# Kernel tuning notes

Measured on AMD Instinct MI355X. Metric: run time of the kernel, lower is better.

Reference implementation:

```python
import jax, jax.numpy as jnp
import numpy as np

TIME_STEP = 7
B, C, D, H, W = 1, 3, 128, 160, 128


def grid_sample_3d(vol, grid):
    """Trilinear grid_sample, padding_mode='border', align_corners=True.
    vol: [B,C,D,H,W]; grid: [B,D,H,W,3] with last dim (x,y,z) in [-1,1]."""
    b, c, d, h, w = vol.shape
    # unnormalize (align_corners=True) and clamp to volume (border padding)
    ix = jnp.clip((grid[..., 0] + 1.0) * 0.5 * (w - 1), 0.0, w - 1)
    iy = jnp.clip((grid[..., 1] + 1.0) * 0.5 * (h - 1), 0.0, h - 1)
    iz = jnp.clip((grid[..., 2] + 1.0) * 0.5 * (d - 1), 0.0, d - 1)

    x0f = jnp.floor(ix); y0f = jnp.floor(iy); z0f = jnp.floor(iz)
    wx = (ix - x0f).reshape(b, 1, -1)
    wy = (iy - y0f).reshape(b, 1, -1)
    wz = (iz - z0f).reshape(b, 1, -1)

    x0 = x0f.astype(jnp.int32); x1 = jnp.minimum(x0 + 1, w - 1)
    y0 = y0f.astype(jnp.int32); y1 = jnp.minimum(y0 + 1, h - 1)
    z0 = z0f.astype(jnp.int32); z1 = jnp.minimum(z0 + 1, d - 1)

    vol_flat = vol.reshape(b, c, d * h * w)

    def gather(zi, yi, xi):
        idx = ((zi * h + yi) * w + xi).reshape(b, 1, -1)  # [B,1,N]
        return jnp.take_along_axis(vol_flat, idx, axis=2)  # [B,C,N]

    out = (gather(z0, y0, x0) * (1 - wz) * (1 - wy) * (1 - wx)
         + gather(z0, y0, x1) * (1 - wz) * (1 - wy) * wx
         + gather(z0, y1, x0) * (1 - wz) * wy * (1 - wx)
         + gather(z0, y1, x1) * (1 - wz) * wy * wx
         + gather(z1, y0, x0) * wz * (1 - wy) * (1 - wx)
         + gather(z1, y0, x1) * wz * (1 - wy) * wx
         + gather(z1, y1, x0) * wz * wy * (1 - wx)
         + gather(z1, y1, x1) * wz * wy * wx)
    return out.reshape(b, c, d, h, w)


def setup_inputs() -> dict:
    key = jax.random.key(0)
    k1, = jax.random.split(key, 1)
    velocity = jax.random.normal(k1, (B, C, D, H, W), dtype=jnp.float32)
    # identity sampling grid, normalized to [-1,1], last dim order (x,y,z)
    gz, gy, gx = jnp.meshgrid(
        jnp.linspace(-1.0, 1.0, D, dtype=jnp.float32),
        jnp.linspace(-1.0, 1.0, H, dtype=jnp.float32),
        jnp.linspace(-1.0, 1.0, W, dtype=jnp.float32),
        indexing='ij')
    sample_grid = jnp.broadcast_to(jnp.stack([gx, gy, gz], axis=-1)[None], (B, D, H, W, 3))
    range_flow = jnp.asarray(0.4, dtype=jnp.float32)
    return {"velocity": velocity, "sample_grid": sample_grid, "range_flow": range_flow}


def reference(velocity, sample_grid, range_flow):
    flow = velocity / (2.0 ** TIME_STEP)
    for _ in range(TIME_STEP):
        grid = sample_grid + jnp.transpose(flow, (0, 2, 3, 4, 1)) * range_flow
        flow = flow + grid_sample_3d(flow, grid)
    return flow
```

## Files before the change

### kernel.cpp

```cpp
#include <hip/hip_runtime.h>


constexpr int D = 128, H = 160, W = 128;
constexpr int N = D * H * W;
constexpr int HC = H / 2, WC = W / 2;
constexpr int NBLK = (D / 2) * (H / 2) * (W / 64);
constexpr int NUM_XCD = 8;
constexpr int CHUNKS_PER_XCD = NBLK / NUM_XCD;

struct alignas(4) f2 { float a, b; };

__device__ __forceinline__ int cube_idx(int z, int y, int x) {
    return ((((z >> 1) * HC + (y >> 1)) * WC + (x >> 1)) << 3)
         | ((z & 1) << 2) | ((y & 1) << 1) | (x & 1);
}

template <bool SRC_PLANAR, bool DST_PLANAR>
__global__ __launch_bounds__(256)
void diffeo_step(const void* __restrict__ src_raw,
                 const float* __restrict__ rf_p,
                 void* __restrict__ dst_raw)
{
    const int b   = blockIdx.x;
    const int xcd = b & (NUM_XCD - 1);
    const int k   = b >> 3;
    const int vb  = xcd * CHUNKS_PER_XCD + k;

    const int zc  = vb / (HC * 2);
    const int rem = vb - zc * (HC * 2);
    const int yc  = rem >> 1;
    const int xh  = rem & 1;

    const int t = threadIdx.x;
    const int x = (xh << 6) | (t & 63);
    const int y = (yc << 1) | ((t >> 6) & 1);
    const int z = (zc << 1) | (t >> 7);

    const float rf = rf_p[0];
    const float s  = 1.0f / 128.0f;

    float3 f;
    if (SRC_PLANAR) {
        const float* sp = (const float*)src_raw;
        const int i = (z * H + y) * W + x;
        f = make_float3(sp[i] * s, sp[i + N] * s, sp[i + 2 * N] * s);
    } else {
        const float4 v = ((const float4*)src_raw)[cube_idx(z, y, x)];
        f = make_float3(v.x, v.y, v.z);
    }

    const float ix = fminf(fmaxf((float)x + f.x * (rf * 0.5f * (float)(W - 1)), 0.0f), (float)(W - 1));
    const float iy = fminf(fmaxf((float)y + f.y * (rf * 0.5f * (float)(H - 1)), 0.0f), (float)(H - 1));
    const float iz = fminf(fmaxf((float)z + f.z * (rf * 0.5f * (float)(D - 1)), 0.0f), (float)(D - 1));

    const float x0f = floorf(ix), y0f = floorf(iy), z0f = floorf(iz);
    const float wx = ix - x0f, wy = iy - y0f, wz = iz - z0f;
    const int x0 = (int)x0f, y0 = (int)y0f, z0 = (int)z0f;
    const int y1 = min(y0 + 1, H - 1);
    const int z1 = min(z0 + 1, D - 1);

    float3 p0[4], p1[4];

    if (SRC_PLANAR) {
        const float* sp = (const float*)src_raw;
        const int xb = min(x0, W - 2);
        const bool hix = (x0 == W - 1);
        int ofs[4];
        ofs[0] = (z0 * H + y0) * W + xb;
        ofs[1] = (z0 * H + y1) * W + xb;
        ofs[2] = (z1 * H + y0) * W + xb;
        ofs[3] = (z1 * H + y1) * W + xb;
#pragma unroll
        for (int q = 0; q < 4; ++q) {
            const f2 px = *(const f2*)(sp + ofs[q]);
            const f2 py = *(const f2*)(sp + N + ofs[q]);
            const f2 pz = *(const f2*)(sp + 2 * N + ofs[q]);
            p0[q] = make_float3(px.a * s, py.a * s, pz.a * s);
            p1[q] = make_float3(px.b * s, py.b * s, pz.b * s);
        }
        if (hix) {
#pragma unroll
            for (int q = 0; q < 4; ++q) p0[q] = p1[q];
        }
    } else {
        const float4* sc = (const float4*)src_raw;
        const int x1 = min(x0 + 1, W - 1);
#pragma unroll
        for (int q = 0; q < 4; ++q) {
            const int zi = (q & 2) ? z1 : z0;
            const int yi = (q & 1) ? y1 : y0;
            const float4 a  = sc[cube_idx(zi, yi, x0)];
            const float4 bq = sc[cube_idx(zi, yi, x1)];
            p0[q] = make_float3(a.x, a.y, a.z);
            p1[q] = make_float3(bq.x, bq.y, bq.z);
        }
    }

    const float omx = 1.0f - wx, omy = 1.0f - wy, omz = 1.0f - wz;
    const float w00 = omz * omy, w01 = omz * wy, w10 = wz * omy, w11 = wz * wy;

    const float vx = w00 * (omx * p0[0].x + wx * p1[0].x)
                   + w01 * (omx * p0[1].x + wx * p1[1].x)
                   + w10 * (omx * p0[2].x + wx * p1[2].x)
                   + w11 * (omx * p0[3].x + wx * p1[3].x);
    const float vy = w00 * (omx * p0[0].y + wx * p1[0].y)
                   + w01 * (omx * p0[1].y + wx * p1[1].y)
                   + w10 * (omx * p0[2].y + wx * p1[2].y)
                   + w11 * (omx * p0[3].y + wx * p1[3].y);
    const float vz = w00 * (omx * p0[0].z + wx * p1[0].z)
                   + w01 * (omx * p0[1].z + wx * p1[1].z)
                   + w10 * (omx * p0[2].z + wx * p1[2].z)
                   + w11 * (omx * p0[3].z + wx * p1[3].z);

    const float o0 = f.x + vx, o1 = f.y + vy, o2 = f.z + vz;

    if (DST_PLANAR) {
        float* __restrict__ dp = (float*)dst_raw;
        const int i = (z * H + y) * W + x;
        dp[i] = o0; dp[i + N] = o1; dp[i + 2 * N] = o2;
    } else {
        ((float4*)dst_raw)[cube_idx(z, y, x)] = make_float4(o0, o1, o2, 0.0f);
    }
}

extern "C" void kernel_launch(void* const* d_in, const int* in_sizes, int n_in,
                              void* d_out, int out_size, void* d_ws, size_t ws_size,
                              hipStream_t stream)
{
    const float* vel = (const float*)d_in[0];
    const float* rf  = (const float*)d_in[2];

    float4* A = (float4*)d_ws;
    float4* B = (float4*)((char*)d_ws + (size_t)48 * 1024 * 1024);

    const dim3 blk(256);
    const dim3 grd(NBLK);

    diffeo_step<true , false><<<grd, blk, 0, stream>>>(vel, rf, A);
    diffeo_step<false, false><<<grd, blk, 0, stream>>>(A,   rf, B);
    diffeo_step<false, false><<<grd, blk, 0, stream>>>(B,   rf, A);
    diffeo_step<false, false><<<grd, blk, 0, stream>>>(A,   rf, B);
    diffeo_step<false, false><<<grd, blk, 0, stream>>>(B,   rf, A);
    diffeo_step<false, false><<<grd, blk, 0, stream>>>(A,   rf, B);
    diffeo_step<false, true ><<<grd, blk, 0, stream>>>(B,   rf, d_out);
}
```

Baseline: 360.2 us.

## Replace Morton-cube float4 layout with linear packed float3 intermediate layout

Intermediate flow buffers change from a 2x2x2-cube-blocked float4 layout to a plain linear array of packed float3. Each 256-thread block now covers a contiguous run of voxels, and the gathers index by linear offset with x and x+1 as adjacent elements. This cuts per-voxel storage from 16 to 12 bytes and drops the cube index arithmetic, at the cost of unaligned 12-byte accesses and less locality in y and z for the trilinear neighbours. The final planar output now uses nontemporal stores.

```diff
diff --git a/kernel.cpp b/kernel.cpp
--- a/kernel.cpp
+++ b/kernel.cpp
@@ -3,17 +3,11 @@
 
 constexpr int D = 128, H = 160, W = 128;
 constexpr int N = D * H * W;
-constexpr int HC = H / 2, WC = W / 2;
-constexpr int NBLK = (D / 2) * (H / 2) * (W / 64);
+constexpr int VOX_BLOCKS = N / 256;
 constexpr int NUM_XCD = 8;
-constexpr int CHUNKS_PER_XCD = NBLK / NUM_XCD;
+constexpr int CHUNKS_PER_XCD = VOX_BLOCKS / NUM_XCD;
 
 struct alignas(4) f2 { float a, b; };
-
-__device__ __forceinline__ int cube_idx(int z, int y, int x) {
-    return ((((z >> 1) * HC + (y >> 1)) * WC + (x >> 1)) << 3)
-         | ((z & 1) << 2) | ((y & 1) << 1) | (x & 1);
-}
 
 template <bool SRC_PLANAR, bool DST_PLANAR>
 __global__ __launch_bounds__(256)
@@ -25,28 +19,22 @@
     const int xcd = b & (NUM_XCD - 1);
     const int k   = b >> 3;
     const int vb  = xcd * CHUNKS_PER_XCD + k;
-
-    const int zc  = vb / (HC * 2);
-    const int rem = vb - zc * (HC * 2);
-    const int yc  = rem >> 1;
-    const int xh  = rem & 1;
-
-    const int t = threadIdx.x;
-    const int x = (xh << 6) | (t & 63);
-    const int y = (yc << 1) | ((t >> 6) & 1);
-    const int z = (zc << 1) | (t >> 7);
+    const int i   = vb * 256 + threadIdx.x;
 
     const float rf = rf_p[0];
     const float s  = 1.0f / 128.0f;
 
+    const int x = i & (W - 1);
+    const int r = i >> 7;
+    const int y = r % H;
+    const int z = r / H;
+
     float3 f;
     if (SRC_PLANAR) {
         const float* sp = (const float*)src_raw;
-        const int i = (z * H + y) * W + x;
         f = make_float3(sp[i] * s, sp[i + N] * s, sp[i + 2 * N] * s);
     } else {
-        const float4 v = ((const float4*)src_raw)[cube_idx(z, y, x)];
-        f = make_float3(v.x, v.y, v.z);
+        f = ((const float3*)src_raw)[i];
     }
 
     const float ix = fminf(fmaxf((float)x + f.x * (rf * 0.5f * (float)(W - 1)), 0.0f), (float)(W - 1));
@@ -59,17 +47,18 @@
     const int y1 = min(y0 + 1, H - 1);
     const int z1 = min(z0 + 1, D - 1);
 
+    const int xb = min(x0, W - 2);
+    const bool hix = (x0 == W - 1);
+
+    int ofs[4];
+    ofs[0] = (z0 * H + y0) * W + xb;
+    ofs[1] = (z0 * H + y1) * W + xb;
+    ofs[2] = (z1 * H + y0) * W + xb;
+    ofs[3] = (z1 * H + y1) * W + xb;
+
     float3 p0[4], p1[4];
-
     if (SRC_PLANAR) {
         const float* sp = (const float*)src_raw;
-        const int xb = min(x0, W - 2);
-        const bool hix = (x0 == W - 1);
-        int ofs[4];
-        ofs[0] = (z0 * H + y0) * W + xb;
-        ofs[1] = (z0 * H + y1) * W + xb;
-        ofs[2] = (z1 * H + y0) * W + xb;
-        ofs[3] = (z1 * H + y1) * W + xb;
 #pragma unroll
         for (int q = 0; q < 4; ++q) {
             const f2 px = *(const f2*)(sp + ofs[q]);
@@ -78,22 +67,17 @@
             p0[q] = make_float3(px.a * s, py.a * s, pz.a * s);
             p1[q] = make_float3(px.b * s, py.b * s, pz.b * s);
         }
-        if (hix) {
-#pragma unroll
-            for (int q = 0; q < 4; ++q) p0[q] = p1[q];
-        }
     } else {
-        const float4* sc = (const float4*)src_raw;
-        const int x1 = min(x0 + 1, W - 1);
+        const float3* s3 = (const float3*)src_raw;
 #pragma unroll
         for (int q = 0; q < 4; ++q) {
-            const int zi = (q & 2) ? z1 : z0;
-            const int yi = (q & 1) ? y1 : y0;
-            const float4 a  = sc[cube_idx(zi, yi, x0)];
-            const float4 bq = sc[cube_idx(zi, yi, x1)];
-            p0[q] = make_float3(a.x, a.y, a.z);
-            p1[q] = make_float3(bq.x, bq.y, bq.z);
+            p0[q] = s3[ofs[q]];
+            p1[q] = s3[ofs[q] + 1];
         }
+    }
+    if (hix) {
+#pragma unroll
+        for (int q = 0; q < 4; ++q) p0[q] = p1[q];
     }
 
     const float omx = 1.0f - wx, omy = 1.0f - wy, omz = 1.0f - wz;
@@ -116,10 +100,11 @@
 
     if (DST_PLANAR) {
         float* __restrict__ dp = (float*)dst_raw;
-        const int i = (z * H + y) * W + x;
-        dp[i] = o0; dp[i + N] = o1; dp[i + 2 * N] = o2;
+        __builtin_nontemporal_store(o0, dp + i);
+        __builtin_nontemporal_store(o1, dp + i + N);
+        __builtin_nontemporal_store(o2, dp + i + 2 * N);
     } else {
-        ((float4*)dst_raw)[cube_idx(z, y, x)] = make_float4(o0, o1, o2, 0.0f);
+        ((float3*)dst_raw)[i] = make_float3(o0, o1, o2);
     }
 }
 
@@ -130,11 +115,11 @@
     const float* vel = (const float*)d_in[0];
     const float* rf  = (const float*)d_in[2];
 
-    float4* A = (float4*)d_ws;
-    float4* B = (float4*)((char*)d_ws + (size_t)48 * 1024 * 1024);
+    float3* A = (float3*)d_ws;
+    float3* B = (float3*)((char*)d_ws + (size_t)48 * 1024 * 1024);
 
     const dim3 blk(256);
-    const dim3 grd(NBLK);
+    const dim3 grd(VOX_BLOCKS);
 
     diffeo_step<true , false><<<grd, blk, 0, stream>>>(vel, rf, A);
     diffeo_step<false, false><<<grd, blk, 0, stream>>>(A,   rf, B);
```

New measurement: 301.4 us. 1.2x faster.
